# Optimization experiments

Hardware: AMD Instinct MI355X
Metric: run time of the kernel (lower is better)

## Reference

```python
import jax, jax.numpy as jnp
import numpy as np

N, E, G, D, H, EMB, L = 200000, 3200000, 4096, 64, 64, 128, 3


def setup_inputs() -> dict:
    key = jax.random.key(0)
    ks = jax.random.split(key, 16)
    s = 0.05
    inp = {}
    inp["x_a"] = jax.random.normal(ks[0], (N, D), jnp.float32)
    inp["edge_index"] = jax.random.randint(ks[1], (2, E), 0, N)
    inp["batch"] = jnp.sort(jax.random.randint(ks[2], (N,), 0, G))
    inp["acid_idx"] = jax.random.randint(ks[3], (G,), 0, 2)
    inp["concentration"] = jax.random.uniform(ks[4], (G,), jnp.float32)
    inp["num_graphs"] = G
    # GIN MLP params per layer (input_dim_a == hl_size == 64, so stackable)
    inp["W1s"] = jax.random.normal(ks[5], (L, D, H), jnp.float32) * s
    inp["b1s"] = jnp.zeros((L, H), jnp.float32)
    inp["gammas"] = jnp.ones((L, H), jnp.float32)
    inp["betas"] = jnp.zeros((L, H), jnp.float32)
    inp["bn_means"] = jnp.zeros((L, H), jnp.float32)   # eval-mode running stats
    inp["bn_vars"] = jnp.ones((L, H), jnp.float32)
    inp["W2s"] = jax.random.normal(ks[6], (L, H, H), jnp.float32) * s
    inp["b2s"] = jnp.zeros((L, H), jnp.float32)
    inp["emb_acid"] = jax.random.normal(ks[7], (2, EMB), jnp.float32)
    inp["emb_conc"] = jax.random.normal(ks[8], (2, EMB), jnp.float32)
    FC_IN = H * L + 2 * EMB  # 448
    inp["fc1_W"] = jax.random.normal(ks[9], (FC_IN, H), jnp.float32) * s
    inp["fc1_b"] = jnp.zeros((H,), jnp.float32)
    inp["fc2_W"] = jax.random.normal(ks[10], (H, 2), jnp.float32) * s
    inp["fc2_b"] = jnp.zeros((2,), jnp.float32)
    return inp


def reference(x_a, edge_index, batch, acid_idx, concentration, num_graphs,
              W1s, b1s, gammas, betas, bn_means, bn_vars, W2s, b2s,
              emb_acid, emb_conc, fc1_W, fc1_b, fc2_W, fc2_b):
    src, dst = edge_index[0], edge_index[1]
    n_nodes = x_a.shape[0]
    x = x_a
    pooled = []
    for l in range(W1s.shape[0]):  # structurally distinct layers (params differ)
        # GINConv, eps=0: MLP(x + sum_{j->i} x_j)
        agg = jax.ops.segment_sum(x[src], dst, num_segments=n_nodes)
        h = x + agg
        h = h @ W1s[l] + b1s[l]
        # BatchNorm1d in eval mode (running stats)
        h = (h - bn_means[l]) * jax.lax.rsqrt(bn_vars[l] + 1e-5) * gammas[l] + betas[l]
        h = jax.nn.relu(h)
        h = jax.nn.relu(h @ W2s[l] + b2s[l])
        x = h  # dropout inactive at eval
        pooled.append(jax.ops.segment_sum(x, batch, num_segments=num_graphs))
    xg = jnp.concatenate(pooled, axis=1)  # [G, L*H]
    conc_idx = jnp.where(concentration == 0.5, 0, 1)
    feat = jnp.concatenate([xg, emb_acid[acid_idx], emb_conc[conc_idx]], axis=1)
    h = jax.nn.relu(feat @ fc1_W + fc1_b)  # dropout inactive at eval
    out = jax.nn.sigmoid(h @ fc2_W + fc2_b)
    return out
```

## Files before the change

kernel.cpp:

```cpp
#include <hip/hip_runtime.h>
#include <math.h>


static __device__ __forceinline__ float rlf(float v, int k) {
    return __int_as_float(__builtin_amdgcn_readlane(__float_as_int(v), k));
}


__global__ void k_hist(const int* __restrict__ dst, int* __restrict__ deg, int E) {
    int i = blockIdx.x * blockDim.x + threadIdx.x;
    int stride = gridDim.x * blockDim.x;
    for (; i < E; i += stride) atomicAdd(&deg[__builtin_nontemporal_load(&dst[i])], 1);
}

#define SCAN_B 512

__global__ void k_scan1(const int* __restrict__ deg, int* __restrict__ ex,
                        int* __restrict__ bsum, int n) {
    __shared__ int s[SCAN_B];
    int t = threadIdx.x;
    int i = blockIdx.x * SCAN_B + t;
    int v = (i < n) ? deg[i] : 0;
    s[t] = v;
    __syncthreads();
    for (int off = 1; off < SCAN_B; off <<= 1) {
        int tv = (t >= off) ? s[t - off] : 0;
        __syncthreads();
        s[t] += tv;
        __syncthreads();
    }
    if (i < n) ex[i] = s[t] - v;
    if (t == SCAN_B - 1) bsum[blockIdx.x] = s[t];
}

__global__ void k_scan2(int* __restrict__ bsum, int nb) {
    __shared__ int s[SCAN_B];
    int t = threadIdx.x;
    int v = (t < nb) ? bsum[t] : 0;
    s[t] = v;
    __syncthreads();
    for (int off = 1; off < SCAN_B; off <<= 1) {
        int tv = (t >= off) ? s[t - off] : 0;
        __syncthreads();
        s[t] += tv;
        __syncthreads();
    }
    if (t < nb) bsum[t] = s[t] - v;
}

__global__ void k_scan3(int* __restrict__ ex, const int* __restrict__ bsum,
                        int n, int E) {
    int i = blockIdx.x * SCAN_B + threadIdx.x;
    if (i < n) ex[i] += bsum[blockIdx.x];
    if (blockIdx.x == 0 && threadIdx.x == 0) ex[n] = E;
}

__global__ void k_scatter(const int* __restrict__ src, const int* __restrict__ dst,
                          const int* __restrict__ row_start, int* __restrict__ cur,
                          int* __restrict__ csr, int E) {
    int i = blockIdx.x * blockDim.x + threadIdx.x;
    int stride = gridDim.x * blockDim.x;
    for (; i < E; i += stride) {
        int d = __builtin_nontemporal_load(&dst[i]);
        int s = __builtin_nontemporal_load(&src[i]);
        int p = atomicAdd(&cur[d], 1);
        __builtin_nontemporal_store(s, &csr[row_start[d] + p]);
    }
}

__global__ void k_gstart(const int* __restrict__ batch, int* __restrict__ gs,
                         int n, int G) {
    int g = blockIdx.x * blockDim.x + threadIdx.x;
    if (g > G) return;
    if (g == G) { gs[G] = n; return; }
    int lo = 0, hi = n;
    while (lo < hi) {
        int mid = (lo + hi) >> 1;
        if (batch[mid] < g) lo = mid + 1; else hi = mid;
    }
    gs[g] = lo;
}

__global__ void k_wt(const float* __restrict__ W, float* __restrict__ Wt, int total) {
    int i = blockIdx.x * blockDim.x + threadIdx.x;
    if (i >= total) return;
    int l = i >> 12, r = i & 4095, j = r >> 6, k = r & 63;
    Wt[(l << 12) + (j << 6) + k] = W[(l << 12) + (k << 6) + j];
}


__global__ __launch_bounds__(256) void k_gather(
    const float* __restrict__ x, const int* __restrict__ row_start,
    const int* __restrict__ csr, float* __restrict__ agg, int n)
{
    int lane = threadIdx.x & 63;
    int g = lane >> 4;
    int c16 = lane & 15;
    int wid = (blockIdx.x * blockDim.x + threadIdx.x) >> 6;
    int nw = (gridDim.x * blockDim.x) >> 6;

    for (int node = wid; node < n; node += nw) {
        int s0 = row_start[node], s1 = row_start[node + 1];
        float4 x4 = *(const float4*)&x[(size_t)node * 64 + c16 * 4];
        float4 acc;
        acc.x = g == 0 ? x4.x : 0.f;
        acc.y = g == 0 ? x4.y : 0.f;
        acc.z = g == 0 ? x4.z : 0.f;
        acc.w = g == 0 ? x4.w : 0.f;

        int j = s0;
        for (; j + 32 <= s1; j += 32) {
            int iA0 = csr[j + g +  0];
            int iA1 = csr[j + g +  4];
            int iA2 = csr[j + g +  8];
            int iA3 = csr[j + g + 12];
            int iB0 = csr[j + g + 16];
            int iB1 = csr[j + g + 20];
            int iB2 = csr[j + g + 24];
            int iB3 = csr[j + g + 28];
            float4 a0 = *(const float4*)&x[(size_t)iA0 * 64 + c16 * 4];
            float4 a1 = *(const float4*)&x[(size_t)iA1 * 64 + c16 * 4];
            float4 a2 = *(const float4*)&x[(size_t)iA2 * 64 + c16 * 4];
            float4 a3 = *(const float4*)&x[(size_t)iA3 * 64 + c16 * 4];
            float4 b0 = *(const float4*)&x[(size_t)iB0 * 64 + c16 * 4];
            float4 b1 = *(const float4*)&x[(size_t)iB1 * 64 + c16 * 4];
            float4 b2 = *(const float4*)&x[(size_t)iB2 * 64 + c16 * 4];
            float4 b3 = *(const float4*)&x[(size_t)iB3 * 64 + c16 * 4];
            acc.x += ((a0.x + a1.x) + (a2.x + a3.x)) + ((b0.x + b1.x) + (b2.x + b3.x));
            acc.y += ((a0.y + a1.y) + (a2.y + a3.y)) + ((b0.y + b1.y) + (b2.y + b3.y));
            acc.z += ((a0.z + a1.z) + (a2.z + a3.z)) + ((b0.z + b1.z) + (b2.z + b3.z));
            acc.w += ((a0.w + a1.w) + (a2.w + a3.w)) + ((b0.w + b1.w) + (b2.w + b3.w));
        }
        if (j + 16 <= s1) {
            int i0 = csr[j + g +  0];
            int i1 = csr[j + g +  4];
            int i2 = csr[j + g +  8];
            int i3 = csr[j + g + 12];
            float4 a0 = *(const float4*)&x[(size_t)i0 * 64 + c16 * 4];
            float4 a1 = *(const float4*)&x[(size_t)i1 * 64 + c16 * 4];
            float4 a2 = *(const float4*)&x[(size_t)i2 * 64 + c16 * 4];
            float4 a3 = *(const float4*)&x[(size_t)i3 * 64 + c16 * 4];
            acc.x += (a0.x + a1.x) + (a2.x + a3.x);
            acc.y += (a0.y + a1.y) + (a2.y + a3.y);
            acc.z += (a0.z + a1.z) + (a2.z + a3.z);
            acc.w += (a0.w + a1.w) + (a2.w + a3.w);
            j += 16;
        }
        int cnt = s1 - j;
        if (cnt) {
#pragma unroll
            for (int u = 0; u < 4; ++u) {
                int p = g + 4 * u;
                int idx = csr[j + (p < cnt ? p : 0)];
                float4 a = *(const float4*)&x[(size_t)idx * 64 + c16 * 4];
                if (p < cnt) {
                    acc.x += a.x; acc.y += a.y; acc.z += a.z; acc.w += a.w;
                }
            }
        }
        acc.x += __shfl_xor(acc.x, 16); acc.y += __shfl_xor(acc.y, 16);
        acc.z += __shfl_xor(acc.z, 16); acc.w += __shfl_xor(acc.w, 16);
        acc.x += __shfl_xor(acc.x, 32); acc.y += __shfl_xor(acc.y, 32);
        acc.z += __shfl_xor(acc.z, 32); acc.w += __shfl_xor(acc.w, 32);
        if (lane < 16)
            *(float4*)&agg[(size_t)node * 64 + c16 * 4] = acc;
    }
}


__global__ __launch_bounds__(256, 2) void k_gemm_pool(
    float* __restrict__ xb,
    const int* __restrict__ gs,
    const float* __restrict__ Wt1, const float* __restrict__ b1,
    const float* __restrict__ gamma, const float* __restrict__ beta,
    const float* __restrict__ mean, const float* __restrict__ var,
    const float* __restrict__ Wt2, const float* __restrict__ b2,
    float* __restrict__ pooled, int G, int lay, int lh)
{
    int lane = threadIdx.x & 63;
    int wid = (blockIdx.x * blockDim.x + threadIdx.x) >> 6;
    if (wid >= G) return;

    float4 w1v[16], w2v[16];
    const float4* W1p = (const float4*)Wt1 + (size_t)lane * 16;
    const float4* W2p = (const float4*)Wt2 + (size_t)lane * 16;
#pragma unroll
    for (int q = 0; q < 16; ++q) w1v[q] = W1p[q];
#pragma unroll
    for (int q = 0; q < 16; ++q) w2v[q] = W2p[q];
#pragma unroll
    for (int q = 0; q < 16; ++q) {
        asm volatile("" : "+v"(w1v[q].x), "+v"(w1v[q].y), "+v"(w1v[q].z), "+v"(w1v[q].w));
        asm volatile("" : "+v"(w2v[q].x), "+v"(w2v[q].y), "+v"(w2v[q].z), "+v"(w2v[q].w));
    }

    float bias1 = b1[lane];
    float sc = gamma[lane] * rsqrtf(var[lane] + 1e-5f);
    float sh = beta[lane] - mean[lane] * sc;
    float bias2 = b2[lane];

    int s0 = gs[wid], s1 = gs[wid + 1];
    int g4 = lane >> 4, c16 = lane & 15;
    float pacc = 0.f;

    for (int nb = s0; nb < s1; nb += 4) {
        int rowc = nb + g4; if (rowc > s1 - 1) rowc = s1 - 1;
        float4 a4 = *(const float4*)&xb[(size_t)rowc * 64 + c16 * 4];

#pragma unroll
        for (int r = 0; r < 4; ++r) {
            if (nb + r >= s1) break;
            float h0 = bias1, h1 = 0.f, h2 = 0.f, h3 = 0.f;
#pragma unroll
            for (int q = 0; q < 16; ++q) {
                h0 += rlf(a4.x, r * 16 + q) * w1v[q].x;
                h1 += rlf(a4.y, r * 16 + q) * w1v[q].y;
                h2 += rlf(a4.z, r * 16 + q) * w1v[q].z;
                h3 += rlf(a4.w, r * 16 + q) * w1v[q].w;
            }
            float h = fmaxf(((h0 + h1) + (h2 + h3)) * sc + sh, 0.f);
            float o0 = bias2, o1 = 0.f, o2 = 0.f, o3 = 0.f;
#pragma unroll
            for (int q = 0; q < 16; ++q) {
                o0 += rlf(h, 4 * q + 0) * w2v[q].x;
                o1 += rlf(h, 4 * q + 1) * w2v[q].y;
                o2 += rlf(h, 4 * q + 2) * w2v[q].z;
                o3 += rlf(h, 4 * q + 3) * w2v[q].w;
            }
            float o = fmaxf((o0 + o1) + (o2 + o3), 0.f);
            xb[(size_t)(nb + r) * 64 + lane] = o;
            pacc += o;
        }
    }
    pooled[(size_t)wid * lh + lay * 64 + lane] = pacc;
}


__global__ __launch_bounds__(256) void k_fc(
    const float* __restrict__ pooled, const int* __restrict__ acid,
    const float* __restrict__ conc, const float* __restrict__ emb_acid,
    const float* __restrict__ emb_conc, const float* __restrict__ fc1W,
    const float* __restrict__ fc1b, const float* __restrict__ fc2W,
    const float* __restrict__ fc2b, float* __restrict__ out, int G, int lh)
{
    __shared__ float sf[4][448];
    int lane = threadIdx.x & 63;
    int w = threadIdx.x >> 6;
    int g = blockIdx.x * 4 + w;
    int fcin = lh + 256;
    if (g < G) {
        const float* pr = pooled + (size_t)g * lh;
        for (int c = lane; c < lh; c += 64) sf[w][c] = pr[c];
        const float* ea = emb_acid + acid[g] * 128;
        int ci = (conc[g] == 0.5f) ? 0 : 1;
        const float* ec = emb_conc + ci * 128;
        sf[w][lh + lane] = ea[lane];
        sf[w][lh + 64 + lane] = ea[lane + 64];
        sf[w][lh + 128 + lane] = ec[lane];
        sf[w][lh + 192 + lane] = ec[lane + 64];
    }
    __syncthreads();
    if (g >= G) return;
    float h0 = fc1b[lane], h1 = 0.f;
    for (int k = 0; k + 2 <= fcin; k += 2) {
        h0 += sf[w][k] * fc1W[(size_t)k * 64 + lane];
        h1 += sf[w][k + 1] * fc1W[(size_t)(k + 1) * 64 + lane];
    }
    float h = fmaxf(h0 + h1, 0.f);
    float p0 = h * fc2W[lane * 2 + 0];
    float p1 = h * fc2W[lane * 2 + 1];
    for (int off = 32; off; off >>= 1) {
        p0 += __shfl_xor(p0, off, 64);
        p1 += __shfl_xor(p1, off, 64);
    }
    if (lane == 0) {
        out[g * 2 + 0] = 1.0f / (1.0f + expf(-(p0 + fc2b[0])));
        out[g * 2 + 1] = 1.0f / (1.0f + expf(-(p1 + fc2b[1])));
    }
}


extern "C" void kernel_launch(void* const* d_in, const int* in_sizes, int n_in,
                              void* d_out, int out_size, void* d_ws, size_t ws_size,
                              hipStream_t stream)
{
    const float* x_a      = (const float*)d_in[0];
    const int*   ei       = (const int*)d_in[1];
    const int*   batch    = (const int*)d_in[2];
    const int*   acid     = (const int*)d_in[3];
    const float* conc     = (const float*)d_in[4];
    const float* W1s      = (const float*)d_in[6];
    const float* b1s      = (const float*)d_in[7];
    const float* gammas   = (const float*)d_in[8];
    const float* betas    = (const float*)d_in[9];
    const float* bn_means = (const float*)d_in[10];
    const float* bn_vars  = (const float*)d_in[11];
    const float* W2s      = (const float*)d_in[12];
    const float* b2s      = (const float*)d_in[13];
    const float* emb_acid = (const float*)d_in[14];
    const float* emb_conc = (const float*)d_in[15];
    const float* fc1W     = (const float*)d_in[16];
    const float* fc1b     = (const float*)d_in[17];
    const float* fc2W     = (const float*)d_in[18];
    const float* fc2b     = (const float*)d_in[19];

    const int N = in_sizes[0] / 64;
    const int E = in_sizes[1] / 2;
    const int G = in_sizes[3];
    const int L = in_sizes[6] / (64 * 64);
    const int LH = 64 * L;

    char* ws = (char*)d_ws;
    size_t off = 0;
    auto alloc = [&](size_t bytes) -> void* {
        void* p = ws + off;
        off += (bytes + 255) & ~(size_t)255;
        return p;
    };
    float* buf0      = (float*)alloc(((size_t)N + 8) * 64 * 4);
    float* buf1      = (float*)alloc(((size_t)N + 8) * 64 * 4);
    float* pooled    = (float*)alloc((size_t)G * LH * 4);
    int*   row_start = (int*)alloc((size_t)(N + 1) * 4);
    int*   deg       = (int*)alloc((size_t)N * 4);
    int*   csr       = (int*)alloc((size_t)E * 4);
    int*   bsum      = (int*)alloc(4096);
    int*   gs        = (int*)alloc((size_t)(G + 1) * 4);
    float* Wt1       = (float*)alloc((size_t)L * 4096 * 4);
    float* Wt2       = (float*)alloc((size_t)L * 4096 * 4);

    const int* srcv = ei;
    const int* dstv = ei + E;

    hipMemsetAsync(deg, 0, (size_t)N * 4, stream);
    k_hist<<<4096, 256, 0, stream>>>(dstv, deg, E);
    int nb = (N + SCAN_B - 1) / SCAN_B;
    k_scan1<<<nb, SCAN_B, 0, stream>>>(deg, row_start, bsum, N);
    k_scan2<<<1, SCAN_B, 0, stream>>>(bsum, nb);
    k_scan3<<<nb, SCAN_B, 0, stream>>>(row_start, bsum, N, E);
    hipMemsetAsync(deg, 0, (size_t)N * 4, stream);
    k_scatter<<<4096, 256, 0, stream>>>(srcv, dstv, row_start, deg, csr, E);
    k_gstart<<<(G + 256) / 256, 256, 0, stream>>>(batch, gs, N, G);

    int wtot = L * 4096;
    k_wt<<<(wtot + 255) / 256, 256, 0, stream>>>(W1s, Wt1, wtot);
    k_wt<<<(wtot + 255) / 256, 256, 0, stream>>>(W2s, Wt2, wtot);

    const float* xin = x_a;
    float* bufs[2] = {buf0, buf1};
    for (int l = 0; l < L; ++l) {
        float* xb = bufs[l & 1];
        k_gather<<<4096, 256, 0, stream>>>(xin, row_start, csr, xb, N);
        k_gemm_pool<<<(G + 3) / 4, 256, 0, stream>>>(
            xb, gs,
            Wt1 + (size_t)l * 4096, b1s + l * 64,
            gammas + l * 64, betas + l * 64,
            bn_means + l * 64, bn_vars + l * 64,
            Wt2 + (size_t)l * 4096, b2s + l * 64,
            pooled, G, l, LH);
        xin = xb;
    }

    k_fc<<<(G + 3) / 4, 256, 0, stream>>>(pooled, acid, conc, emb_acid, emb_conc,
                                          fc1W, fc1b, fc2W, fc2b,
                                          (float*)d_out, G, LH);
}
```

Before: 1.243 ms.

## Partition CSR histogram and scatter atomics by XCD-owned destination ranges

The histogram and scatter kernels now assign each of eight block groups (selected by blockIdx & 7, which matches round-robin XCD dispatch) a contiguous eighth of the destination node range. Each group scans every edge but only does atomics for destinations it owns, so the atomic targets stay in one XCD's L2 and cross-XCD coherence traffic goes away. The cost is that each group re-reads the whole dst array, eight times the index reads in total. The scatter store also drops the nontemporal hint.

```diff
diff --git a/kernel.cpp b/kernel.cpp
--- a/kernel.cpp
+++ b/kernel.cpp
@@ -7,10 +7,19 @@
 }
 
 
-__global__ void k_hist(const int* __restrict__ dst, int* __restrict__ deg, int E) {
-    int i = blockIdx.x * blockDim.x + threadIdx.x;
-    int stride = gridDim.x * blockDim.x;
-    for (; i < E; i += stride) atomicAdd(&deg[__builtin_nontemporal_load(&dst[i])], 1);
+__global__ void k_hist(const int* __restrict__ dst, int* __restrict__ deg,
+                       int E, int n) {
+    int xcd = blockIdx.x & 7;
+    int gblk = blockIdx.x >> 3;
+    int nblk = gridDim.x >> 3;
+    int lo = (int)((long long)n * xcd / 8);
+    int hi = (int)((long long)n * (xcd + 1) / 8);
+    int i = gblk * blockDim.x + threadIdx.x;
+    int stride = nblk * blockDim.x;
+    for (; i < E; i += stride) {
+        int d = __builtin_nontemporal_load(&dst[i]);
+        if (d >= lo && d < hi) atomicAdd(&deg[d], 1);
+    }
 }
 
 #define SCAN_B 512
@@ -57,14 +66,21 @@
 
 __global__ void k_scatter(const int* __restrict__ src, const int* __restrict__ dst,
                           const int* __restrict__ row_start, int* __restrict__ cur,
-                          int* __restrict__ csr, int E) {
-    int i = blockIdx.x * blockDim.x + threadIdx.x;
-    int stride = gridDim.x * blockDim.x;
+                          int* __restrict__ csr, int E, int n) {
+    int xcd = blockIdx.x & 7;
+    int gblk = blockIdx.x >> 3;
+    int nblk = gridDim.x >> 3;
+    int lo = (int)((long long)n * xcd / 8);
+    int hi = (int)((long long)n * (xcd + 1) / 8);
+    int i = gblk * blockDim.x + threadIdx.x;
+    int stride = nblk * blockDim.x;
     for (; i < E; i += stride) {
         int d = __builtin_nontemporal_load(&dst[i]);
-        int s = __builtin_nontemporal_load(&src[i]);
-        int p = atomicAdd(&cur[d], 1);
-        __builtin_nontemporal_store(s, &csr[row_start[d] + p]);
+        if (d >= lo && d < hi) {
+            int s = __builtin_nontemporal_load(&src[i]);
+            int p = atomicAdd(&cur[d], 1);
+            csr[row_start[d] + p] = s;
+        }
     }
 }
 
@@ -332,13 +348,13 @@
     const int* dstv = ei + E;
 
     hipMemsetAsync(deg, 0, (size_t)N * 4, stream);
-    k_hist<<<4096, 256, 0, stream>>>(dstv, deg, E);
+    k_hist<<<4096, 256, 0, stream>>>(dstv, deg, E, N);
     int nb = (N + SCAN_B - 1) / SCAN_B;
     k_scan1<<<nb, SCAN_B, 0, stream>>>(deg, row_start, bsum, N);
     k_scan2<<<1, SCAN_B, 0, stream>>>(bsum, nb);
     k_scan3<<<nb, SCAN_B, 0, stream>>>(row_start, bsum, N, E);
     hipMemsetAsync(deg, 0, (size_t)N * 4, stream);
-    k_scatter<<<4096, 256, 0, stream>>>(srcv, dstv, row_start, deg, csr, E);
+    k_scatter<<<4096, 256, 0, stream>>>(srcv, dstv, row_start, deg, csr, E, N);
     k_gstart<<<(G + 256) / 256, 256, 0, stream>>>(batch, gs, N, G);
 
     int wtot = L * 4096;
```

After: 1.216 ms. 2.2% less time.
